# Performance work log

Hardware: AMD Instinct MI355X
Metric: run time of the kernel (lower is better)

Reference implementation:

```python
import jax, jax.numpy as jnp
import numpy as np

N = 100000       # nodes
E = 1600000      # edges (before self-loops)
IN = 32          # input_dim
HID = 64         # hidden_dim
HEADS = 4
HO = HID // HEADS  # per-head out of gat1
OUT = 32         # output_dim
HID2 = HID // 2
BN_EPS = 1e-5
NEG_SLOPE = 0.2  # PyG GATConv default leaky relu slope


def setup_inputs() -> dict:
    key = jax.random.key(0)
    ks = jax.random.split(key, 28)
    f32 = jnp.float32
    rn = lambda k, s, sc=0.1: jax.random.normal(k, s, f32) * sc
    inp = {}
    inp["x"] = jax.random.normal(ks[0], (N, IN), f32)
    inp["edge_index"] = jax.random.randint(ks[1], (2, E), 0, N, jnp.int32)
    # GATConv 1: in=IN, heads=HEADS, out/head=HO, concat
    inp["W1"] = rn(ks[2], (IN, HEADS * HO))
    inp["att_src1"] = rn(ks[3], (HEADS, HO))
    inp["att_dst1"] = rn(ks[4], (HEADS, HO))
    inp["b1"] = rn(ks[5], (HEADS * HO,))
    # GATConv 2: in=HID, heads=1, out=OUT, no concat (mean)
    inp["W2"] = rn(ks[6], (HID, OUT))
    inp["att_src2"] = rn(ks[7], (1, OUT))
    inp["att_dst2"] = rn(ks[8], (1, OUT))
    inp["b2"] = rn(ks[9], (OUT,))
    # BatchNorms (inference mode: running stats)
    inp["bn1_g"] = jnp.ones((HID,), f32)
    inp["bn1_b"] = jnp.zeros((HID,), f32)
    inp["bn1_m"] = rn(ks[10], (HID,), 0.1)
    inp["bn1_v"] = jax.random.uniform(ks[11], (HID,), f32, 0.5, 1.5)
    inp["bn2_g"] = jnp.ones((OUT,), f32)
    inp["bn2_b"] = jnp.zeros((OUT,), f32)
    inp["bn2_m"] = rn(ks[12], (OUT,), 0.1)
    inp["bn2_v"] = jax.random.uniform(ks[13], (OUT,), f32, 0.5, 1.5)
    # classifier: OUT -> HID2 -> 3
    inp["cls_w1"] = rn(ks[14], (OUT, HID2))
    inp["cls_b1"] = rn(ks[15], (HID2,))
    inp["cls_w2"] = rn(ks[16], (HID2, 3))
    inp["cls_b2"] = rn(ks[17], (3,))
    inp["reg_w1"] = rn(ks[18], (OUT, HID2))
    inp["reg_b1"] = rn(ks[19], (HID2,))
    inp["reg_w2"] = rn(ks[20], (HID2, 1))
    inp["reg_b2"] = rn(ks[21], (1,))
    return inp


def _segment_softmax(e, seg, n):
    # e: [E, H]; softmax over edges sharing the same destination segment
    m = jax.ops.segment_max(e, seg, num_segments=n)
    ex = jnp.exp(e - m[seg])
    s = jax.ops.segment_sum(ex, seg, num_segments=n)
    return ex / (s[seg] + 1e-16)


def _gat(x, src, dst, W, a_src, a_dst, b, heads, ho, concat):
    n = x.shape[0]
    h = (x @ W).reshape(n, heads, ho)                    # [N,H,F]
    e = (h * a_src).sum(-1)[src] + (h * a_dst).sum(-1)[dst]  # [E,H]
    e = jax.nn.leaky_relu(e, NEG_SLOPE)
    alpha = _segment_softmax(e, dst, n)                  # [E,H]
    out = jax.ops.segment_sum(h[src] * alpha[:, :, None], dst, num_segments=n)
    out = out.reshape(n, heads * ho) if concat else out.mean(axis=1)
    return out + b


def _bn(x, g, b, m, v):
    return (x - m) * jax.lax.rsqrt(v + BN_EPS) * g + b


def reference(x, edge_index, W1, att_src1, att_dst1, b1, W2, att_src2, att_dst2, b2,
              bn1_g, bn1_b, bn1_m, bn1_v, bn2_g, bn2_b, bn2_m, bn2_v,
              cls_w1, cls_b1, cls_w2, cls_b2, reg_w1, reg_b1, reg_w2, reg_b2):
    n = x.shape[0]
    # PyG GATConv default add_self_loops=True
    loops = jnp.arange(n, dtype=edge_index.dtype)
    src = jnp.concatenate([edge_index[0], loops])
    dst = jnp.concatenate([edge_index[1], loops])

    h = _gat(x, src, dst, W1, att_src1, att_dst1, b1, HEADS, HO, True)   # [N, HID]
    h = jax.nn.relu(_bn(h, bn1_g, bn1_b, bn1_m, bn1_v))
    emb = _gat(h, src, dst, W2, att_src2, att_dst2, b2, 1, OUT, False)   # [N, OUT]
    emb = jax.nn.relu(_bn(emb, bn2_g, bn2_b, bn2_m, bn2_v))

    roles = jax.nn.relu(emb @ cls_w1 + cls_b1) @ cls_w2 + cls_b2          # [N, 3]
    energy = jax.nn.relu(emb @ reg_w1 + reg_b1) @ reg_w2 + reg_b2         # [N, 1]
    return emb, roles, energy
```

## Files before the change

kernel.cpp:

```cpp
#include <hip/hip_runtime.h>
#include <hip/hip_bf16.h>

#define NN 100000
#define EE 1600000
#define ETOT (EE + NN)
#define IND 32
#define HIDD 64
#define NHEADS 4
#define OUTD 32
#define HID2D 32

#define BSH 9
#define NBUCK 196
#define CAP 10240
#define EPB 2048

typedef unsigned int uint;

__device__ __forceinline__ uint pack2(float a, float b) {
  uint lo = (uint)__bfloat16_as_ushort(__float2bfloat16(a));
  uint hi = (uint)__bfloat16_as_ushort(__float2bfloat16(b));
  return (hi << 16) | lo;
}
__device__ __forceinline__ float lo2f(uint w) { return __uint_as_float(w << 16); }
__device__ __forceinline__ float hi2f(uint w) { return __uint_as_float(w & 0xFFFF0000u); }

__global__ __launch_bounds__(256) void k_lin1(
    const float* __restrict__ x, const float* __restrict__ W1,
    const float* __restrict__ atsrc, const float* __restrict__ atdst,
    uint* __restrict__ h1u, float* __restrict__ as1, float* __restrict__ ad1) {
  __shared__ float Ws[IND * HIDD];
  __shared__ float xs[8 * IND];
  __shared__ float atS[HIDD], atD[HIDD];
  int t = threadIdx.x;
  for (int i = t; i < IND * HIDD; i += 256) Ws[i] = W1[i];
  if (t < HIDD) { atS[t] = atsrc[t]; atD[t] = atdst[t]; }
  xs[t] = x[blockIdx.x * 256 + t];
  __syncthreads();
  int nl = t >> 5, tl = t & 31;
  int node = blockIdx.x * 8 + nl;
  int j0 = 2 * tl, j1 = j0 + 1;
  float a0 = 0.f, a1 = 0.f;
#pragma unroll
  for (int k = 0; k < IND; k++) {
    float xv = xs[nl * IND + k];
    a0 += xv * Ws[k * HIDD + j0];
    a1 += xv * Ws[k * HIDD + j1];
  }
  h1u[node * 32 + tl] = pack2(a0, a1);
  float ps = a0 * atS[j0] + a1 * atS[j1];
  float pd = a0 * atD[j0] + a1 * atD[j1];
#pragma unroll
  for (int off = 4; off >= 1; off >>= 1) {
    ps += __shfl_down(ps, off, 8);
    pd += __shfl_down(pd, off, 8);
  }
  if ((tl & 7) == 0) {
    as1[node * NHEADS + (tl >> 3)] = ps;
    ad1[node * NHEADS + (tl >> 3)] = pd;
  }
}

__global__ __launch_bounds__(256) void k_lin2(
    const float* __restrict__ hbn, const float* __restrict__ W2,
    const float* __restrict__ atsrc, const float* __restrict__ atdst,
    uint* __restrict__ h2u, float* __restrict__ as2, float* __restrict__ ad2) {
  __shared__ float Ws[HIDD * OUTD];
  __shared__ float xs[16 * HIDD];
  __shared__ float atS[OUTD], atD[OUTD];
  int t = threadIdx.x;
  for (int i = t; i < HIDD * OUTD; i += 256) Ws[i] = W2[i];
  if (t < OUTD) { atS[t] = atsrc[t]; atD[t] = atdst[t]; }
  for (int i = t; i < 16 * HIDD; i += 256) xs[i] = hbn[blockIdx.x * 16 * HIDD + i];
  __syncthreads();
  int nl = t >> 4, tl = t & 15;
  int node = blockIdx.x * 16 + nl;
  int j0 = 2 * tl, j1 = j0 + 1;
  float a0 = 0.f, a1 = 0.f;
#pragma unroll
  for (int k = 0; k < HIDD; k++) {
    float xv = xs[nl * HIDD + k];
    a0 += xv * Ws[k * OUTD + j0];
    a1 += xv * Ws[k * OUTD + j1];
  }
  h2u[node * 16 + tl] = pack2(a0, a1);
  float ps = a0 * atS[j0] + a1 * atS[j1];
  float pd = a0 * atD[j0] + a1 * atD[j1];
#pragma unroll
  for (int off = 8; off >= 1; off >>= 1) {
    ps += __shfl_down(ps, off, 16);
    pd += __shfl_down(pd, off, 16);
  }
  if (tl == 0) { as2[node] = ps; ad2[node] = pd; }
}

__global__ __launch_bounds__(256) void k_bin(const int* __restrict__ ei,
                                             int* __restrict__ bcur,
                                             int* __restrict__ bins) {
  __shared__ int cnt[NBUCK];
  int t = threadIdx.x;
  for (int i = t; i < NBUCK; i += 256) cnt[i] = 0;
  __syncthreads();
  int base = blockIdx.x * EPB;
  int recs[8], bks[8];
#pragma unroll
  for (int k = 0; k < 8; k++) {
    int i = base + k * 256 + t;
    recs[k] = -1; bks[k] = 0;
    if (i < ETOT) {
      int s, d;
      if (i < EE) { s = ei[i]; d = ei[EE + i]; } else { s = i - EE; d = s; }
      recs[k] = (s << BSH) | (d & ((1 << BSH) - 1));
      bks[k] = d >> BSH;
      atomicAdd(&cnt[bks[k]], 1);
    }
  }
  __syncthreads();
  for (int i = t; i < NBUCK; i += 256) cnt[i] = atomicAdd(&bcur[i], cnt[i]);
  __syncthreads();
#pragma unroll
  for (int k = 0; k < 8; k++) {
    if (recs[k] >= 0) {
      int pos = atomicAdd(&cnt[bks[k]], 1);
      bins[bks[k] * CAP + pos] = recs[k];
    }
  }
}

__global__ __launch_bounds__(256) void k_csr(const int* __restrict__ bcur,
                                             const int* __restrict__ bins,
                                             int* __restrict__ rowp,
                                             int* __restrict__ srcs) {
  __shared__ int lrec[CAP];
  __shared__ int ldeg[512], sA[512], sB[512];
  int b = blockIdx.x, t = threadIdx.x;
  sA[t] = (t < NBUCK) ? bcur[t] : 0;
  __syncthreads();
  int* in = sA; int* out = sB;
  for (int off = 1; off < 256; off <<= 1) {
    out[t] = in[t] + ((t >= off) ? in[t - off] : 0);
    __syncthreads();
    int* tmp = in; in = out; out = tmp;
  }
  int gb = (b == 0) ? 0 : in[b - 1];
  if (b == 0 && t == 0) rowp[NN] = ETOT;
  __syncthreads();
  int count = bcur[b]; if (count > CAP) count = CAP;
  for (int i = t; i < 512; i += 256) ldeg[i] = 0;
  __syncthreads();
  for (int i = t; i < count; i += 256) {
    int r = bins[b * CAP + i];
    lrec[i] = r;
    atomicAdd(&ldeg[r & 511], 1);
  }
  __syncthreads();
  for (int i = t; i < 512; i += 256) sA[i] = ldeg[i];
  __syncthreads();
  in = sA; out = sB;
  for (int off = 1; off < 512; off <<= 1) {
    for (int i = t; i < 512; i += 256)
      out[i] = in[i] + ((i >= off) ? in[i - off] : 0);
    __syncthreads();
    int* tmp = in; in = out; out = tmp;
  }
  int nb = b << BSH;
  for (int i = t; i < 512; i += 256) {
    int ex = in[i] - ldeg[i];
    if (nb + i < NN) rowp[nb + i] = gb + ex;
    ldeg[i] = ex;
  }
  __syncthreads();
  for (int i = t; i < count; i += 256) {
    int r = lrec[i];
    int pos = atomicAdd(&ldeg[r & 511], 1);
    srcs[gb + pos] = r >> BSH;
  }
}

__global__ __launch_bounds__(256) void k_agg1(
    const int* __restrict__ rowp, const int* __restrict__ srcs,
    const uint* __restrict__ h1u, const float* __restrict__ as1,
    const float* __restrict__ ad1, const float* __restrict__ b1,
    const float* __restrict__ g, const float* __restrict__ bb,
    const float* __restrict__ m, const float* __restrict__ v,
    float* __restrict__ hbn) {
  int t = threadIdx.x;
  int wid = t >> 6, lane = t & 63;
  int nA = blockIdx.x * 8 + wid * 2;
  int nB = nA + 1;
  int slot = lane >> 3;
  int fl = lane & 7;
  int hd = fl >> 1;
  int stA = rowp[nA], eA = rowp[nA + 1], eB = rowp[nB + 1];
  int stB = eA;
  int lpA = eA - 1, lpB = eB - 1;
  float advA = ad1[nA * NHEADS + hd];
  float advB = ad1[nB * NHEADS + hd];
  const uint4* h14 = (const uint4*)h1u;
  float accA[8] = {0,0,0,0,0,0,0,0}, accB[8] = {0,0,0,0,0,0,0,0};
  float lA = 0.f, lB = 0.f;
  int pA = stA + slot, pB = stB + slot;
  int sA0 = srcs[pA < lpA ? pA : lpA];
  int sB0 = srcs[pB < lpB ? pB : lpB];
  uint4 wA = h14[sA0 * 8 + fl];
  uint4 wB = h14[sB0 * 8 + fl];
  float asA = as1[sA0 * NHEADS + hd];
  float asB = as1[sB0 * NHEADS + hd];
  int p1A = pA + 8, p1B = pB + 8;
  int sA1 = srcs[p1A < lpA ? p1A : lpA];
  int sB1 = srcs[p1B < lpB ? p1B : lpB];
  while (pA < eA || pB < eB) {
    uint4 wnA = h14[sA1 * 8 + fl];
    uint4 wnB = h14[sB1 * 8 + fl];
    float anA = as1[sA1 * NHEADS + hd];
    float anB = as1[sB1 * NHEADS + hd];
    int p2A = p1A + 8, p2B = p1B + 8;
    int sA2 = srcs[p2A < lpA ? p2A : lpA];
    int sB2 = srcs[p2B < lpB ? p2B : lpB];
    if (pA < eA) {
      float e = asA + advA;
      e = fmaxf(e, 0.2f * e);
      float ex = __expf(e);
      lA += ex;
      accA[0] += ex * lo2f(wA.x); accA[1] += ex * hi2f(wA.x);
      accA[2] += ex * lo2f(wA.y); accA[3] += ex * hi2f(wA.y);
      accA[4] += ex * lo2f(wA.z); accA[5] += ex * hi2f(wA.z);
      accA[6] += ex * lo2f(wA.w); accA[7] += ex * hi2f(wA.w);
    }
    if (pB < eB) {
      float e = asB + advB;
      e = fmaxf(e, 0.2f * e);
      float ex = __expf(e);
      lB += ex;
      accB[0] += ex * lo2f(wB.x); accB[1] += ex * hi2f(wB.x);
      accB[2] += ex * lo2f(wB.y); accB[3] += ex * hi2f(wB.y);
      accB[4] += ex * lo2f(wB.z); accB[5] += ex * hi2f(wB.z);
      accB[6] += ex * lo2f(wB.w); accB[7] += ex * hi2f(wB.w);
    }
    wA = wnA; wB = wnB; asA = anA; asB = anB;
    sA1 = sA2; sB1 = sB2;
    pA = p1A; pB = p1B; p1A = p2A; p1B = p2B;
  }
#pragma unroll
  for (int off = 8; off <= 32; off <<= 1) {
#pragma unroll
    for (int i = 0; i < 8; i++) {
      accA[i] += __shfl_xor(accA[i], off, 64);
      accB[i] += __shfl_xor(accB[i], off, 64);
    }
    lA += __shfl_xor(lA, off, 64);
    lB += __shfl_xor(lB, off, 64);
  }
  if (slot < 2) {
    int node = slot == 0 ? nA : nB;
    float lsum = slot == 0 ? lA : lB;
    float li = 1.f / (lsum + 1e-16f);
    int fb = fl * 8;
    float o[8];
#pragma unroll
    for (int i = 0; i < 8; i++) {
      int j = fb + i;
      float av = slot == 0 ? accA[i] : accB[i];
      float ov = av * li + b1[j];
      ov = (ov - m[j]) * rsqrtf(v[j] + 1e-5f) * g[j] + bb[j];
      o[i] = fmaxf(ov, 0.f);
    }
    float4* dst = (float4*)(hbn + node * HIDD + fb);
    dst[0] = make_float4(o[0], o[1], o[2], o[3]);
    dst[1] = make_float4(o[4], o[5], o[6], o[7]);
  }
}

__global__ __launch_bounds__(256) void k_agg2(
    const int* __restrict__ rowp, const int* __restrict__ srcs,
    const uint* __restrict__ h2u, const float* __restrict__ as2,
    const float* __restrict__ ad2, const float* __restrict__ b2v,
    const float* __restrict__ g, const float* __restrict__ bb,
    const float* __restrict__ m, const float* __restrict__ v,
    float* __restrict__ out_emb) {
  int t = threadIdx.x;
  int wid = t >> 6, lane = t & 63;
  int node = blockIdx.x * 4 + wid;
  int slot = lane >> 3;
  int fl = lane & 7;
  int start = rowp[node], end = rowp[node + 1];
  int lastp = end - 1;
  float adv = ad2[node];
  const uint2* h22 = (const uint2*)h2u;
  float acc[4] = {0.f, 0.f, 0.f, 0.f};
  float l = 0.f;
  int p = start + slot;
  int pc = p < lastp ? p : lastp;
  int s0 = srcs[pc];
  uint2 w = h22[s0 * 8 + fl];
  float as = as2[s0];
  int p1 = p + 8;
  int pc1 = p1 < lastp ? p1 : lastp;
  int s1 = srcs[pc1];
  while (p < end) {
    uint2 wn = h22[s1 * 8 + fl];
    float asn = as2[s1];
    int p2 = p1 + 8;
    int pc2 = p2 < lastp ? p2 : lastp;
    int s2 = srcs[pc2];
    float e = as + adv;
    e = fmaxf(e, 0.2f * e);
    float ex = __expf(e);
    l += ex;
    acc[0] += ex * lo2f(w.x); acc[1] += ex * hi2f(w.x);
    acc[2] += ex * lo2f(w.y); acc[3] += ex * hi2f(w.y);
    w = wn; as = asn; s1 = s2; p = p1; p1 = p2;
  }
#pragma unroll
  for (int off = 8; off <= 32; off <<= 1) {
#pragma unroll
    for (int i = 0; i < 4; i++) acc[i] += __shfl_xor(acc[i], off, 64);
    l += __shfl_xor(l, off, 64);
  }
  if (slot == 0) {
    float li = 1.f / (l + 1e-16f);
    int fb = fl * 4;
    float o[4];
#pragma unroll
    for (int i = 0; i < 4; i++) {
      int j = fb + i;
      float ov = acc[i] * li + b2v[j];
      ov = (ov - m[j]) * rsqrtf(v[j] + 1e-5f) * g[j] + bb[j];
      o[i] = fmaxf(ov, 0.f);
    }
    *(float4*)(out_emb + node * OUTD + fb) = make_float4(o[0], o[1], o[2], o[3]);
  }
}

__global__ __launch_bounds__(256) void k_mlp(
    const float* __restrict__ embf,
    const float* __restrict__ cw1, const float* __restrict__ cb1,
    const float* __restrict__ cw2, const float* __restrict__ cb2,
    const float* __restrict__ rw1, const float* __restrict__ rb1,
    const float* __restrict__ rw2, const float* __restrict__ rb2,
    float* __restrict__ out_roles, float* __restrict__ out_energy) {
  __shared__ float C1[OUTD * HID2D], R1[OUTD * HID2D];
  __shared__ float C2[HID2D * 3], CB1[HID2D], RB1[HID2D], R2[HID2D];
  __shared__ float CB2v[3], RB2v;
  int t = threadIdx.x;
  for (int i = t; i < OUTD * HID2D; i += 256) { C1[i] = cw1[i]; R1[i] = rw1[i]; }
  if (t < HID2D) { CB1[t] = cb1[t]; RB1[t] = rb1[t]; R2[t] = rw2[t]; }
  if (t < HID2D * 3) C2[t] = cw2[t];
  if (t < 3) CB2v[t] = cb2[t];
  if (t == 0) RB2v = rb2[0];
  __syncthreads();
  int node = blockIdx.x * 256 + t;
  if (node >= NN) return;
  float e[OUTD];
#pragma unroll
  for (int k = 0; k < OUTD; k++) e[k] = embf[node * OUTD + k];
  float r0 = CB2v[0], r1 = CB2v[1], r2 = CB2v[2], en = RB2v;
  for (int j = 0; j < HID2D; j++) {
    float hc = CB1[j], hr = RB1[j];
#pragma unroll
    for (int k = 0; k < OUTD; k++) {
      hc += e[k] * C1[k * HID2D + j];
      hr += e[k] * R1[k * HID2D + j];
    }
    hc = fmaxf(hc, 0.f);
    hr = fmaxf(hr, 0.f);
    r0 += hc * C2[j * 3 + 0];
    r1 += hc * C2[j * 3 + 1];
    r2 += hc * C2[j * 3 + 2];
    en += hr * R2[j];
  }
  out_roles[node * 3 + 0] = r0;
  out_roles[node * 3 + 1] = r1;
  out_roles[node * 3 + 2] = r2;
  out_energy[node] = en;
}

extern "C" void kernel_launch(void* const* d_in, const int* in_sizes, int n_in,
                              void* d_out, int out_size, void* d_ws, size_t ws_size,
                              hipStream_t stream) {
  const float* x    = (const float*)d_in[0];
  const int*   ei   = (const int*)d_in[1];
  const float* W1   = (const float*)d_in[2];
  const float* as1w = (const float*)d_in[3];
  const float* ad1w = (const float*)d_in[4];
  const float* b1   = (const float*)d_in[5];
  const float* W2   = (const float*)d_in[6];
  const float* as2w = (const float*)d_in[7];
  const float* ad2w = (const float*)d_in[8];
  const float* b2v  = (const float*)d_in[9];
  const float* bn1g = (const float*)d_in[10];
  const float* bn1b = (const float*)d_in[11];
  const float* bn1m = (const float*)d_in[12];
  const float* bn1v = (const float*)d_in[13];
  const float* bn2g = (const float*)d_in[14];
  const float* bn2b = (const float*)d_in[15];
  const float* bn2m = (const float*)d_in[16];
  const float* bn2v = (const float*)d_in[17];
  const float* cw1  = (const float*)d_in[18];
  const float* cb1  = (const float*)d_in[19];
  const float* cw2  = (const float*)d_in[20];
  const float* cb2  = (const float*)d_in[21];
  const float* rw1  = (const float*)d_in[22];
  const float* rb1  = (const float*)d_in[23];
  const float* rw2  = (const float*)d_in[24];
  const float* rb2  = (const float*)d_in[25];

  uint*  h1u = (uint*)d_ws;
  float* hbn = (float*)(h1u + NN * 32);
  float* as1 = hbn + NN * HIDD;
  float* ad1 = as1 + NN * NHEADS;
  int* rowp  = (int*)(ad1 + NN * NHEADS);
  int* srcs  = rowp + NN + 1;
  int* bcur  = srcs + ETOT;
  int* bins  = bcur + 256;
  uint* h2u  = h1u;
  float* as2 = as1;
  float* ad2 = ad1;

  float* out        = (float*)d_out;
  float* out_emb    = out;
  float* out_roles  = out + NN * OUTD;
  float* out_energy = out + NN * (OUTD + 3);

  hipMemsetAsync(bcur, 0, NBUCK * sizeof(int), stream);
  k_bin<<<(ETOT + EPB - 1) / EPB, 256, 0, stream>>>(ei, bcur, bins);
  k_csr<<<NBUCK, 256, 0, stream>>>(bcur, bins, rowp, srcs);
  k_lin1<<<NN / 8, 256, 0, stream>>>(x, W1, as1w, ad1w, h1u, as1, ad1);
  k_agg1<<<NN / 8, 256, 0, stream>>>(rowp, srcs, h1u, as1, ad1, b1, bn1g, bn1b, bn1m, bn1v, hbn);
  k_lin2<<<NN / 16, 256, 0, stream>>>(hbn, W2, as2w, ad2w, h2u, as2, ad2);
  k_agg2<<<NN / 4, 256, 0, stream>>>(rowp, srcs, h2u, as2, ad2, b2v, bn2g, bn2b, bn2m, bn2v, out_emb);
  k_mlp<<<(NN + 255) / 256, 256, 0, stream>>>(out_emb, cw1, cb1, cw2, cb2, rw1, rb1, rw2, rb2, out_roles, out_energy);
}
```

Before: 346.5 us.

## Halve CSR bucket size and process two nodes per wave in layer-2 aggregation

The CSR build now uses 256-node buckets (391 blocks, smaller shared record buffer), so more blocks run and each one needs less LDS. The bucket-prefix scan is widened to 512 entries and the local degree scan shrinks to 256. k_agg2 now interleaves two destination nodes per wavefront with independent prefetch chains, which adds memory-level parallelism and halves the block count. The two-node loop adds per-iteration predication, and a bucket that overflows the smaller capacity would silently drop edges.

```diff
diff --git a/kernel.cpp b/kernel.cpp
--- a/kernel.cpp
+++ b/kernel.cpp
@@ -10,9 +10,9 @@
 #define OUTD 32
 #define HID2D 32
 
-#define BSH 9
-#define NBUCK 196
-#define CAP 10240
+#define BSH 8
+#define NBUCK 391
+#define CAP 5120
 #define EPB 2048
 
 typedef unsigned int uint;
@@ -132,47 +132,48 @@
                                              int* __restrict__ rowp,
                                              int* __restrict__ srcs) {
   __shared__ int lrec[CAP];
-  __shared__ int ldeg[512], sA[512], sB[512];
+  __shared__ int sA[512], sB[512];
+  __shared__ int ldeg[256];
   int b = blockIdx.x, t = threadIdx.x;
   sA[t] = (t < NBUCK) ? bcur[t] : 0;
+  sA[t + 256] = (t + 256 < NBUCK) ? bcur[t + 256] : 0;
   __syncthreads();
   int* in = sA; int* out = sB;
-  for (int off = 1; off < 256; off <<= 1) {
-    out[t] = in[t] + ((t >= off) ? in[t - off] : 0);
-    __syncthreads();
-    int* tmp = in; in = out; out = tmp;
-  }
-  int gb = (b == 0) ? 0 : in[b - 1];
-  if (b == 0 && t == 0) rowp[NN] = ETOT;
-  __syncthreads();
-  int count = bcur[b]; if (count > CAP) count = CAP;
-  for (int i = t; i < 512; i += 256) ldeg[i] = 0;
-  __syncthreads();
-  for (int i = t; i < count; i += 256) {
-    int r = bins[b * CAP + i];
-    lrec[i] = r;
-    atomicAdd(&ldeg[r & 511], 1);
-  }
-  __syncthreads();
-  for (int i = t; i < 512; i += 256) sA[i] = ldeg[i];
-  __syncthreads();
-  in = sA; out = sB;
   for (int off = 1; off < 512; off <<= 1) {
     for (int i = t; i < 512; i += 256)
       out[i] = in[i] + ((i >= off) ? in[i - off] : 0);
     __syncthreads();
     int* tmp = in; in = out; out = tmp;
   }
+  int gb = (b == 0) ? 0 : in[b - 1];
+  if (b == 0 && t == 0) rowp[NN] = ETOT;
+  __syncthreads();
+  int count = bcur[b]; if (count > CAP) count = CAP;
+  ldeg[t] = 0;
+  __syncthreads();
+  for (int i = t; i < count; i += 256) {
+    int r = bins[b * CAP + i];
+    lrec[i] = r;
+    atomicAdd(&ldeg[r & 255], 1);
+  }
+  __syncthreads();
+  int dv = ldeg[t];
+  sA[t] = dv;
+  __syncthreads();
+  in = sA; out = sB;
+  for (int off = 1; off < 256; off <<= 1) {
+    out[t] = in[t] + ((t >= off) ? in[t - off] : 0);
+    __syncthreads();
+    int* tmp = in; in = out; out = tmp;
+  }
   int nb = b << BSH;
-  for (int i = t; i < 512; i += 256) {
-    int ex = in[i] - ldeg[i];
-    if (nb + i < NN) rowp[nb + i] = gb + ex;
-    ldeg[i] = ex;
-  }
+  int ex = in[t] - dv;
+  if (nb + t < NN) rowp[nb + t] = gb + ex;
+  ldeg[t] = ex;
   __syncthreads();
   for (int i = t; i < count; i += 256) {
     int r = lrec[i];
-    int pos = atomicAdd(&ldeg[r & 511], 1);
+    int pos = atomicAdd(&ldeg[r & 255], 1);
     srcs[gb + pos] = r >> BSH;
   }
 }
@@ -280,51 +281,74 @@
     float* __restrict__ out_emb) {
   int t = threadIdx.x;
   int wid = t >> 6, lane = t & 63;
-  int node = blockIdx.x * 4 + wid;
+  int nA = blockIdx.x * 8 + wid * 2;
+  int nB = nA + 1;
   int slot = lane >> 3;
   int fl = lane & 7;
-  int start = rowp[node], end = rowp[node + 1];
-  int lastp = end - 1;
-  float adv = ad2[node];
+  int stA = rowp[nA], eA = rowp[nA + 1], eB = rowp[nB + 1];
+  int stB = eA;
+  int lpA = eA - 1, lpB = eB - 1;
+  float advA = ad2[nA], advB = ad2[nB];
   const uint2* h22 = (const uint2*)h2u;
-  float acc[4] = {0.f, 0.f, 0.f, 0.f};
-  float l = 0.f;
-  int p = start + slot;
-  int pc = p < lastp ? p : lastp;
-  int s0 = srcs[pc];
-  uint2 w = h22[s0 * 8 + fl];
-  float as = as2[s0];
-  int p1 = p + 8;
-  int pc1 = p1 < lastp ? p1 : lastp;
-  int s1 = srcs[pc1];
-  while (p < end) {
-    uint2 wn = h22[s1 * 8 + fl];
-    float asn = as2[s1];
-    int p2 = p1 + 8;
-    int pc2 = p2 < lastp ? p2 : lastp;
-    int s2 = srcs[pc2];
-    float e = as + adv;
-    e = fmaxf(e, 0.2f * e);
-    float ex = __expf(e);
-    l += ex;
-    acc[0] += ex * lo2f(w.x); acc[1] += ex * hi2f(w.x);
-    acc[2] += ex * lo2f(w.y); acc[3] += ex * hi2f(w.y);
-    w = wn; as = asn; s1 = s2; p = p1; p1 = p2;
+  float accA[4] = {0,0,0,0}, accB[4] = {0,0,0,0};
+  float lA = 0.f, lB = 0.f;
+  int pA = stA + slot, pB = stB + slot;
+  int sA0 = srcs[pA < lpA ? pA : lpA];
+  int sB0 = srcs[pB < lpB ? pB : lpB];
+  uint2 wA = h22[sA0 * 8 + fl];
+  uint2 wB = h22[sB0 * 8 + fl];
+  float asA = as2[sA0], asB = as2[sB0];
+  int p1A = pA + 8, p1B = pB + 8;
+  int sA1 = srcs[p1A < lpA ? p1A : lpA];
+  int sB1 = srcs[p1B < lpB ? p1B : lpB];
+  while (pA < eA || pB < eB) {
+    uint2 wnA = h22[sA1 * 8 + fl];
+    uint2 wnB = h22[sB1 * 8 + fl];
+    float anA = as2[sA1], anB = as2[sB1];
+    int p2A = p1A + 8, p2B = p1B + 8;
+    int sA2 = srcs[p2A < lpA ? p2A : lpA];
+    int sB2 = srcs[p2B < lpB ? p2B : lpB];
+    if (pA < eA) {
+      float e = asA + advA;
+      e = fmaxf(e, 0.2f * e);
+      float ex = __expf(e);
+      lA += ex;
+      accA[0] += ex * lo2f(wA.x); accA[1] += ex * hi2f(wA.x);
+      accA[2] += ex * lo2f(wA.y); accA[3] += ex * hi2f(wA.y);
+    }
+    if (pB < eB) {
+      float e = asB + advB;
+      e = fmaxf(e, 0.2f * e);
+      float ex = __expf(e);
+      lB += ex;
+      accB[0] += ex * lo2f(wB.x); accB[1] += ex * hi2f(wB.x);
+      accB[2] += ex * lo2f(wB.y); accB[3] += ex * hi2f(wB.y);
+    }
+    wA = wnA; wB = wnB; asA = anA; asB = anB;
+    sA1 = sA2; sB1 = sB2;
+    pA = p1A; pB = p1B; p1A = p2A; p1B = p2B;
   }
 #pragma unroll
   for (int off = 8; off <= 32; off <<= 1) {
 #pragma unroll
-    for (int i = 0; i < 4; i++) acc[i] += __shfl_xor(acc[i], off, 64);
-    l += __shfl_xor(l, off, 64);
-  }
-  if (slot == 0) {
-    float li = 1.f / (l + 1e-16f);
+    for (int i = 0; i < 4; i++) {
+      accA[i] += __shfl_xor(accA[i], off, 64);
+      accB[i] += __shfl_xor(accB[i], off, 64);
+    }
+    lA += __shfl_xor(lA, off, 64);
+    lB += __shfl_xor(lB, off, 64);
+  }
+  if (slot < 2) {
+    int node = slot == 0 ? nA : nB;
+    float lsum = slot == 0 ? lA : lB;
+    float li = 1.f / (lsum + 1e-16f);
     int fb = fl * 4;
     float o[4];
 #pragma unroll
     for (int i = 0; i < 4; i++) {
       int j = fb + i;
-      float ov = acc[i] * li + b2v[j];
+      float av = slot == 0 ? accA[i] : accB[i];
+      float ov = av * li + b2v[j];
       ov = (ov - m[j]) * rsqrtf(v[j] + 1e-5f) * g[j] + bb[j];
       o[i] = fmaxf(ov, 0.f);
     }
@@ -412,7 +436,7 @@
   int* rowp  = (int*)(ad1 + NN * NHEADS);
   int* srcs  = rowp + NN + 1;
   int* bcur  = srcs + ETOT;
-  int* bins  = bcur + 256;
+  int* bins  = bcur + 512;
   uint* h2u  = h1u;
   float* as2 = as1;
   float* ad2 = ad1;
@@ -422,12 +446,12 @@
   float* out_roles  = out + NN * OUTD;
   float* out_energy = out + NN * (OUTD + 3);
 
-  hipMemsetAsync(bcur, 0, NBUCK * sizeof(int), stream);
+  hipMemsetAsync(bcur, 0, 512 * sizeof(int), stream);
   k_bin<<<(ETOT + EPB - 1) / EPB, 256, 0, stream>>>(ei, bcur, bins);
   k_csr<<<NBUCK, 256, 0, stream>>>(bcur, bins, rowp, srcs);
   k_lin1<<<NN / 8, 256, 0, stream>>>(x, W1, as1w, ad1w, h1u, as1, ad1);
   k_agg1<<<NN / 8, 256, 0, stream>>>(rowp, srcs, h1u, as1, ad1, b1, bn1g, bn1b, bn1m, bn1v, hbn);
   k_lin2<<<NN / 16, 256, 0, stream>>>(hbn, W2, as2w, ad2w, h2u, as2, ad2);
-  k_agg2<<<NN / 4, 256, 0, stream>>>(rowp, srcs, h2u, as2, ad2, b2v, bn2g, bn2b, bn2m, bn2v, out_emb);
+  k_agg2<<<NN / 8, 256, 0, stream>>>(rowp, srcs, h2u, as2, ad2, b2v, bn2g, bn2b, bn2m, bn2v, out_emb);
   k_mlp<<<(NN + 255) / 256, 256, 0, stream>>>(out_emb, cw1, cb1, cw2, cb2, rw1, rb1, rw2, rb2, out_roles, out_energy);
 }
```

Result: faster. 326.8 us (-5.7%).
